# Performance work log

Measured on AMD Instinct MI355X. Metric: run time of the kernel, lower is better.

Reference implementation:

```python
import jax, jax.numpy as jnp
import numpy as np

B, S, D, H = 2, 2048, 1024, 16
DK = D // H
EPS = 1e-5


def setup_inputs() -> dict:
    key = jax.random.key(0)
    ks = jax.random.split(key, 6)
    std = (2.0 / (D + D)) ** 0.5
    return {
        "x": jax.random.normal(ks[0], (B, S, D), dtype=jnp.float32),
        "W_Q": jax.random.normal(ks[1], (D, D), dtype=jnp.float32) * std,
        "W_K": jax.random.normal(ks[2], (D, D), dtype=jnp.float32) * std,
        "W_V": jax.random.normal(ks[3], (D, D), dtype=jnp.float32) * std,
        "W_O": jax.random.normal(ks[4], (D, D), dtype=jnp.float32) * std,
        "gain": jnp.ones((D,), dtype=jnp.float32),
        "positions": jnp.arange(S, dtype=jnp.int64 if jax.config.jax_enable_x64 else jnp.int32),
        "theta": 10000,
        "max_seq_len": 2048,
    }


def rmsnorm(x, gain):
    xf = x.astype(jnp.float32)
    rms = jnp.sqrt(jnp.mean(xf * xf, axis=-1, keepdims=True) + EPS)
    return ((xf / rms) * gain).astype(x.dtype)


def apply_rope(x, sin, cos):
    # x: [..., seq, dk]; sin/cos: [seq, dk//2] broadcast over leading dims
    x_even = x[..., 0::2]
    x_odd = x[..., 1::2]
    r_even = x_even * cos - x_odd * sin
    r_odd = x_odd * cos + x_even * sin
    return jnp.stack([r_even, r_odd], axis=-1).reshape(x.shape)


def reference(x, W_Q, W_K, W_V, W_O, gain, positions, theta, max_seq_len):
    seq_len = x.shape[-2]
    Q = jnp.einsum('od,bsd->bso', W_Q, x)
    K = jnp.einsum('od,bsd->bso', W_K, x)
    V = jnp.einsum('od,bsd->bso', W_V, x)
    # RMSNorm over full d_model BEFORE head split (as in original)
    Q = rmsnorm(Q, gain)
    K = rmsnorm(K, gain)
    # split heads: [b, h, s, dk]
    Q = Q.reshape(*Q.shape[:-1], H, DK).swapaxes(-3, -2)
    K = K.reshape(*K.shape[:-1], H, DK).swapaxes(-3, -2)
    V = V.reshape(*V.shape[:-1], H, DK).swapaxes(-3, -2)
    # RoPE tables
    exponents = 2.0 * jnp.arange(DK // 2, dtype=jnp.float32) / DK
    inv_freq = 1.0 / (jnp.float32(theta) ** exponents)
    angles = positions.astype(jnp.float32)[:, None] * inv_freq[None, :]  # [S, DK//2]
    sin, cos = jnp.sin(angles), jnp.cos(angles)
    Q = apply_rope(Q, sin, cos)
    K = apply_rope(K, sin, cos)
    # causal attention
    scores = jnp.einsum('bhqd,bhkd->bhqk', Q, K) / jnp.sqrt(jnp.float32(DK))
    causal = jnp.tril(jnp.ones((seq_len, seq_len), dtype=bool))
    scores = jnp.where(causal, scores, -jnp.inf)
    attn = jax.nn.softmax(scores, axis=-1)
    out = jnp.einsum('bhqk,bhkd->bhqd', attn, V)
    out = out.swapaxes(-3, -2).reshape(*x.shape[:-1], D)
    return jnp.einsum('of,bsf->bso', W_O, out)
```

## Files before the change

kernel.cpp:

```cpp
#include <hip/hip_runtime.h>
#include <hip/hip_bf16.h>

typedef __attribute__((ext_vector_type(8))) __bf16 bf16x8;
typedef __attribute__((ext_vector_type(4))) __bf16 bf16x4;
typedef __attribute__((ext_vector_type(4))) float  f32x4;

#define S_LEN 2048
#define D_DIM 1024
#define NH    16
#define GK    1024
#define GN    1024

__device__ __forceinline__ float fast_exp2(float x) {
#if __has_builtin(__builtin_amdgcn_exp2f)
  return __builtin_amdgcn_exp2f(x);
#else
  return exp2f(x);
#endif
}

__device__ __forceinline__ void gld_lds16(const void* g, void* l) {
  __builtin_amdgcn_global_load_lds(
      (const __attribute__((address_space(1))) unsigned int*)g,
      (__attribute__((address_space(3))) unsigned int*)l, 16, 0, 0);
}

__global__ __launch_bounds__(256) void cast_all(
    const float* __restrict__ x,  const float* __restrict__ wq, const float* __restrict__ wk,
    const float* __restrict__ wv, const float* __restrict__ wo,
    __bf16* __restrict__ xb, __bf16* __restrict__ wqb, __bf16* __restrict__ wkb,
    __bf16* __restrict__ wvb, __bf16* __restrict__ wob)
{
  const int NTOT = 2 << 20;
  for (int i = blockIdx.x * 256 + threadIdx.x; i < NTOT; i += 1024 * 256) {
    const float* s; __bf16* d; int off;
    if (i < (1 << 20)) { s = x; d = xb; off = i; }
    else {
      const int j = i - (1 << 20);
      const int r = j >> 18; off = j & ((1 << 18) - 1);
      s = (r == 0) ? wq : (r == 1) ? wk : (r == 2) ? wv : wo;
      d = (r == 0) ? wqb : (r == 1) ? wkb : (r == 2) ? wvb : wob;
    }
    float4 v = ((const float4*)s)[off];
    bf16x4 o = { (__bf16)v.x, (__bf16)v.y, (__bf16)v.z, (__bf16)v.w };
    ((bf16x4*)d)[off] = o;
  }
}

__global__ __launch_bounds__(256) void gemm_bt(
    const __bf16* __restrict__ A,
    const __bf16* __restrict__ W0, const __bf16* __restrict__ W1, const __bf16* __restrict__ W2,
    __bf16* __restrict__ C0, __bf16* __restrict__ C1, __bf16* __restrict__ VtOut)
{
  const int mode = blockIdx.z;
  const __bf16* Wm = (mode == 0) ? W0 : (mode == 1) ? W1 : W2;

  __shared__ __align__(16) __bf16 As[128 * 64];
  __shared__ __align__(16) __bf16 Bs[128 * 64];

  const int tid  = threadIdx.x;
  const int lane = tid & 63;
  const int w    = tid >> 6;
  const int wr   = w >> 1, wc = w & 1;
  const int lm   = lane & 15, qd = lane >> 4;
  const int m0 = blockIdx.y * 128, n0 = blockIdx.x * 128;

  const __bf16* ap[4]; const __bf16* bp[4]; int lo[4];
  #pragma unroll
  for (int j = 0; j < 4; j++) {
    const int c = tid + 256 * j;
    const int r = c >> 3, cpos = c & 7;
    const int g = (cpos ^ (r & 7)) * 8;
    ap[j] = A  + (size_t)(m0 + r) * GK + g;
    bp[j] = Wm + (size_t)(n0 + r) * GK + g;
    lo[j] = c * 8;
  }

  const int sw = lm & 7;

  f32x4 zero = {0.f, 0.f, 0.f, 0.f};
  f32x4 acc[4][4];
  #pragma unroll
  for (int i = 0; i < 4; i++)
    #pragma unroll
    for (int j = 0; j < 4; j++) acc[i][j] = zero;

  for (int k0 = 0; k0 < GK; k0 += 64) {
    #pragma unroll
    for (int j = 0; j < 4; j++) {
      gld_lds16(ap[j] + k0, &As[lo[j]]);
      gld_lds16(bp[j] + k0, &Bs[lo[j]]);
    }
    __syncthreads();
    #pragma unroll
    for (int half = 0; half < 2; half++) {
      const int cph = ((qd + 4 * half) ^ sw) * 8;
      bf16x8 af[4], bfv[4];
      #pragma unroll
      for (int i = 0; i < 4; i++) af[i]  = *(const bf16x8*)&As[(wr * 64 + i * 16 + lm) * 64 + cph];
      #pragma unroll
      for (int j = 0; j < 4; j++) bfv[j] = *(const bf16x8*)&Bs[(wc * 64 + j * 16 + lm) * 64 + cph];
      #pragma unroll
      for (int i = 0; i < 4; i++)
        #pragma unroll
        for (int j = 0; j < 4; j++)
          acc[i][j] = __builtin_amdgcn_mfma_f32_16x16x32_bf16(af[i], bfv[j], acc[i][j], 0, 0, 0);
    }
    __syncthreads();
  }

  if (mode < 2) {
    __bf16* C = (mode == 0) ? C0 : C1;
    #pragma unroll
    for (int i = 0; i < 4; i++) {
      const int row = m0 + wr * 64 + i * 16 + qd * 4;
      #pragma unroll
      for (int j = 0; j < 4; j++) {
        const int col = n0 + wc * 64 + j * 16 + lm;
        #pragma unroll
        for (int r = 0; r < 4; r++)
          C[(size_t)(row + r) * GN + col] = (__bf16)acc[i][j][r];
      }
    }
  } else {
    #pragma unroll
    for (int i = 0; i < 4; i++) {
      const int row = m0 + wr * 64 + i * 16 + qd * 4;
      const int b = row >> 11, s = row & (S_LEN - 1);
      #pragma unroll
      for (int j = 0; j < 4; j++) {
        const int col = n0 + wc * 64 + j * 16 + lm;
        const int h = col >> 6, d = col & 63;
        bf16x4 o = { (__bf16)acc[i][j][0], (__bf16)acc[i][j][1],
                     (__bf16)acc[i][j][2], (__bf16)acc[i][j][3] };
        *(bf16x4*)(VtOut + (((size_t)(b * NH + h) * 64 + d) * S_LEN + s)) = o;
      }
    }
  }
}

__global__ __launch_bounds__(256) void gemm_out64(
    const __bf16* __restrict__ A, const __bf16* __restrict__ Wm, float* __restrict__ C)
{
  __shared__ __align__(16) __bf16 As[64 * 64];
  __shared__ __align__(16) __bf16 Bs[128 * 64];

  const int tid  = threadIdx.x;
  const int lane = tid & 63;
  const int w    = tid >> 6;
  const int wr   = w >> 1, wc = w & 1;
  const int lm   = lane & 15, qd = lane >> 4;
  const int m0 = blockIdx.y * 64, n0 = blockIdx.x * 128;

  const __bf16* ap[2]; int loA[2];
  #pragma unroll
  for (int j = 0; j < 2; j++) {
    const int c = tid + 256 * j;
    const int r = c >> 3, cpos = c & 7;
    ap[j] = A + (size_t)(m0 + r) * GK + (cpos ^ (r & 7)) * 8;
    loA[j] = c * 8;
  }
  const __bf16* bp[4]; int loB[4];
  #pragma unroll
  for (int j = 0; j < 4; j++) {
    const int c = tid + 256 * j;
    const int r = c >> 3, cpos = c & 7;
    bp[j] = Wm + (size_t)(n0 + r) * GK + (cpos ^ (r & 7)) * 8;
    loB[j] = c * 8;
  }

  const int sw = lm & 7;

  f32x4 zero = {0.f, 0.f, 0.f, 0.f};
  f32x4 acc[2][4];
  #pragma unroll
  for (int i = 0; i < 2; i++)
    #pragma unroll
    for (int j = 0; j < 4; j++) acc[i][j] = zero;

  for (int k0 = 0; k0 < GK; k0 += 64) {
    #pragma unroll
    for (int j = 0; j < 2; j++) gld_lds16(ap[j] + k0, &As[loA[j]]);
    #pragma unroll
    for (int j = 0; j < 4; j++) gld_lds16(bp[j] + k0, &Bs[loB[j]]);
    __syncthreads();
    #pragma unroll
    for (int half = 0; half < 2; half++) {
      const int cph = ((qd + 4 * half) ^ sw) * 8;
      bf16x8 af[2], bfv[4];
      #pragma unroll
      for (int i = 0; i < 2; i++) af[i]  = *(const bf16x8*)&As[(wr * 32 + i * 16 + lm) * 64 + cph];
      #pragma unroll
      for (int j = 0; j < 4; j++) bfv[j] = *(const bf16x8*)&Bs[(wc * 64 + j * 16 + lm) * 64 + cph];
      #pragma unroll
      for (int i = 0; i < 2; i++)
        #pragma unroll
        for (int j = 0; j < 4; j++)
          acc[i][j] = __builtin_amdgcn_mfma_f32_16x16x32_bf16(af[i], bfv[j], acc[i][j], 0, 0, 0);
    }
    __syncthreads();
  }

  #pragma unroll
  for (int i = 0; i < 2; i++) {
    const int row = m0 + wr * 32 + i * 16 + qd * 4;
    #pragma unroll
    for (int j = 0; j < 4; j++) {
      const int col = n0 + wc * 64 + j * 16 + lm;
      #pragma unroll
      for (int r = 0; r < 4; r++)
        C[(size_t)(row + r) * GN + col] = acc[i][j][r];
    }
  }
}

__global__ __launch_bounds__(256) void norm_rope(
    const __bf16* __restrict__ Qf, const __bf16* __restrict__ Kf,
    const float* __restrict__ gain, const int* __restrict__ positions,
    const int* __restrict__ theta_p,
    __bf16* __restrict__ Qh, __bf16* __restrict__ Kh)
{
  const int row = blockIdx.x;
  const int s = row & (S_LEN - 1), b = row >> 11;
  const int t = threadIdx.x, d0 = t * 4;

  const bf16x4 qv = *(const bf16x4*)(Qf + (size_t)row * D_DIM + d0);
  const bf16x4 kv = *(const bf16x4*)(Kf + (size_t)row * D_DIM + d0);
  const float q0 = (float)qv[0], q1 = (float)qv[1], q2 = (float)qv[2], q3 = (float)qv[3];
  const float k0 = (float)kv[0], k1 = (float)kv[1], k2 = (float)kv[2], k3 = (float)kv[3];

  float sq = q0 * q0 + q1 * q1 + q2 * q2 + q3 * q3;
  float sk = k0 * k0 + k1 * k1 + k2 * k2 + k3 * k3;
  #pragma unroll
  for (int off = 32; off; off >>= 1) { sq += __shfl_xor(sq, off); sk += __shfl_xor(sk, off); }
  __shared__ float red[8];
  const int lane = t & 63, wv = t >> 6;
  if (lane == 0) { red[wv] = sq; red[4 + wv] = sk; }
  __syncthreads();
  sq = red[0] + red[1] + red[2] + red[3];
  sk = red[4] + red[5] + red[6] + red[7];
  const float invq = rsqrtf(sq * (1.0f / 1024.0f) + 1e-5f);
  const float invk = rsqrtf(sk * (1.0f / 1024.0f) + 1e-5f);

  const float4 g = *(const float4*)(gain + d0);
  const float qn0 = q0 * invq * g.x, qn1 = q1 * invq * g.y;
  const float qn2 = q2 * invq * g.z, qn3 = q3 * invq * g.w;
  const float kn0 = k0 * invk * g.x, kn1 = k1 * invk * g.y;
  const float kn2 = k2 * invk * g.z, kn3 = k3 * invk * g.w;

  const float pos = (float)positions[s];
  const float th  = (float)theta_p[0];
  const int idx = d0 & 63, h = d0 >> 6, p0 = idx >> 1;
  const float lg32 = __log2f(th) * (1.0f / 32.0f);
  const float f0 = fast_exp2(-(float)p0 * lg32);
  const float f1 = fast_exp2(-(float)(p0 + 1) * lg32);
  float s0, cc0, s1, cc1;
  __sincosf(pos * f0, &s0, &cc0);
  __sincosf(pos * f1, &s1, &cc1);

  const float qe0 = qn0 * cc0 - qn1 * s0, qo0 = qn1 * cc0 + qn0 * s0;
  const float qe1 = qn2 * cc1 - qn3 * s1, qo1 = qn3 * cc1 + qn2 * s1;
  const float ke0 = kn0 * cc0 - kn1 * s0, ko0 = kn1 * cc0 + kn0 * s0;
  const float ke1 = kn2 * cc1 - kn3 * s1, ko1 = kn3 * cc1 + kn2 * s1;

  const size_t obase = ((size_t)((b * NH + h) * S_LEN + s)) * 64 + idx;
  bf16x4 qo = { (__bf16)qe0, (__bf16)qo0, (__bf16)qe1, (__bf16)qo1 };
  bf16x4 ko = { (__bf16)ke0, (__bf16)ko0, (__bf16)ke1, (__bf16)ko1 };
  *(bf16x4*)(Qh + obase) = qo;
  *(bf16x4*)(Kh + obase) = ko;
}

__global__ __launch_bounds__(256) void attn_fwd(
    const __bf16* __restrict__ Qh, const __bf16* __restrict__ Kh,
    const __bf16* __restrict__ Vt, __bf16* __restrict__ Ob)
{
  const int bid = blockIdx.x + 16 * blockIdx.y;
  const int px  = bid >> 5;
  const int rr  = bid & 31;
  const int bh  = (rr & 7) * 4 + (rr >> 3);
  const int tid = threadIdx.x, lane = tid & 63, w = tid >> 6;
  const int lm = lane & 15, qd = lane >> 4;

  __shared__ __align__(16) __bf16 smem[2 * 4096 + 2 * 4096 + 4 * 1152];
  __bf16* Ks = smem;
  __bf16* Vs = smem + 8192;
  __bf16* Pw = smem + 16384 + w * 1152;

  const int qtA = px, qtB = 31 - px;
  const int rowA = qtA * 64 + w * 16, rowB = qtB * 64 + w * 16;

  const size_t qbase = (size_t)bh * S_LEN * 64;
  const bf16x8 aqA0 = *(const bf16x8*)(Qh + qbase + (size_t)(rowA + lm) * 64 + qd * 8);
  const bf16x8 aqA1 = *(const bf16x8*)(Qh + qbase + (size_t)(rowA + lm) * 64 + 32 + qd * 8);
  const bf16x8 aqB0 = *(const bf16x8*)(Qh + qbase + (size_t)(rowB + lm) * 64 + qd * 8);
  const bf16x8 aqB1 = *(const bf16x8*)(Qh + qbase + (size_t)(rowB + lm) * 64 + 32 + qd * 8);

  const __bf16* Kb = Kh + (size_t)bh * S_LEN * 64;
  const __bf16* Vb = Vt + (size_t)bh * 64 * S_LEN;
  const int c0 = tid, c1 = 256 + tid;
  const int kr0 = c0 >> 3, kr1 = c1 >> 3;
  const int kg0 = ((c0 & 7) ^ (kr0 & 7)) * 8;
  const int kg1 = ((c1 & 7) ^ (kr1 & 7)) * 8;
  const int cpA = (qd ^ (lm & 7)) * 8;
  const int cpB = cpA ^ 32;

  auto stage = [&](int buf, int k0) {
    __bf16* Kd = Ks + buf * 4096;
    __bf16* Vd = Vs + buf * 4096;
    gld_lds16(Kb + (size_t)(k0 + kr0) * 64 + kg0, &Kd[c0 * 8]);
    gld_lds16(Kb + (size_t)(k0 + kr1) * 64 + kg1, &Kd[c1 * 8]);
    gld_lds16(Vb + (size_t)kr0 * S_LEN + k0 + kg0, &Vd[c0 * 8]);
    gld_lds16(Vb + (size_t)kr1 * S_LEN + k0 + kg1, &Vd[c1 * 8]);
  };

  const float SC2 = 0.125f * 1.44269504089f;
  const float OFF = 12.0f;
  f32x4 zero = {0.f, 0.f, 0.f, 0.f};
  float l[4];
  f32x4 o[4];

  stage(0, 0);

  const int b = bh >> 4, h = bh & 15;

  for (int it = 0; it < 33; ++it) {
    const int seg = (it > qtA);
    const int kt  = seg ? it - qtA - 1 : it;
    const int qt  = seg ? qtB : qtA;
    const int cur = it & 1;

    if (kt == 0) {
      #pragma unroll
      for (int r = 0; r < 4; r++) l[r] = 0.f;
      #pragma unroll
      for (int jb = 0; jb < 4; jb++) o[jb] = zero;
    }

    __syncthreads();
    if (it + 1 < 33) {
      const int nkt = (it + 1 > qtA) ? it - qtA : it + 1;
      stage(cur ^ 1, nkt * 64);
    }

    const __bf16* Kc = Ks + cur * 4096;
    const __bf16* Vc = Vs + cur * 4096;
    const bf16x8 a0 = seg ? aqB0 : aqA0;
    const bf16x8 a1 = seg ? aqB1 : aqA1;
    const int rowg = (seg ? rowB : rowA) + qd * 4;
    const int k0 = kt * 64;

    float p[4][4];
    const bool diag = (kt == qt);
    #pragma unroll
    for (int kb = 0; kb < 4; kb++) {
      const int krow = (kb * 16 + lm) * 64;
      const bf16x8 bk0 = *(const bf16x8*)&Kc[krow + cpA];
      const bf16x8 bk1 = *(const bf16x8*)&Kc[krow + cpB];
      f32x4 sc = zero;
      sc = __builtin_amdgcn_mfma_f32_16x16x32_bf16(a0, bk0, sc, 0, 0, 0);
      sc = __builtin_amdgcn_mfma_f32_16x16x32_bf16(a1, bk1, sc, 0, 0, 0);
      if (diag) {
        const int colg = k0 + kb * 16 + lm;
        #pragma unroll
        for (int r = 0; r < 4; r++) {
          const float e = fast_exp2(fmaf(sc[r], SC2, -OFF));
          p[kb][r] = (colg <= rowg + r) ? e : 0.f;
          l[r] += p[kb][r];
        }
      } else {
        #pragma unroll
        for (int r = 0; r < 4; r++) {
          p[kb][r] = fast_exp2(fmaf(sc[r], SC2, -OFF));
          l[r] += p[kb][r];
        }
      }
    }

    #pragma unroll
    for (int kb = 0; kb < 4; kb++)
      #pragma unroll
      for (int r = 0; r < 4; r++)
        Pw[(qd * 4 + r) * 72 + kb * 16 + lm] = (__bf16)p[kb][r];

    const bf16x8 ap0 = *(const bf16x8*)&Pw[lm * 72 + qd * 8];
    const bf16x8 ap1 = *(const bf16x8*)&Pw[lm * 72 + 32 + qd * 8];
    #pragma unroll
    for (int jb = 0; jb < 4; jb++) {
      const int vrow = (jb * 16 + lm) * 64;
      const bf16x8 bv0 = *(const bf16x8*)&Vc[vrow + cpA];
      const bf16x8 bv1 = *(const bf16x8*)&Vc[vrow + cpB];
      o[jb] = __builtin_amdgcn_mfma_f32_16x16x32_bf16(ap1, bv1,
              __builtin_amdgcn_mfma_f32_16x16x32_bf16(ap0, bv0, o[jb], 0, 0, 0), 0, 0, 0);
    }

    if (kt == qt) {
      #pragma unroll
      for (int r = 0; r < 4; r++) {
        float lr = l[r];
        #pragma unroll
        for (int off = 8; off; off >>= 1) lr += __shfl_xor(lr, off);
        const float inv = 1.0f / lr;
        const size_t base = ((size_t)(b * S_LEN + rowg + r)) * D_DIM + h * 64;
        #pragma unroll
        for (int jb = 0; jb < 4; jb++)
          Ob[base + jb * 16 + lm] = (__bf16)(o[jb][r] * inv);
      }
    }
  }
}

extern "C" void kernel_launch(void* const* d_in, const int* in_sizes, int n_in,
                              void* d_out, int out_size, void* d_ws, size_t ws_size,
                              hipStream_t stream)
{
  (void)in_sizes; (void)n_in; (void)out_size; (void)ws_size;
  const float* x    = (const float*)d_in[0];
  const float* WQ   = (const float*)d_in[1];
  const float* WK   = (const float*)d_in[2];
  const float* WV   = (const float*)d_in[3];
  const float* WO   = (const float*)d_in[4];
  const float* gain = (const float*)d_in[5];
  const int* positions = (const int*)d_in[6];
  const int* theta     = (const int*)d_in[7];
  float* out = (float*)d_out;

  char* ws = (char*)d_ws;
  const size_t MB = 1024 * 1024;
  __bf16* xb  = (__bf16*)(ws + 0);
  __bf16* WQb = (__bf16*)(ws + 8  * MB);
  __bf16* WKb = (__bf16*)(ws + 10 * MB);
  __bf16* WVb = (__bf16*)(ws + 12 * MB);
  __bf16* WOb = (__bf16*)(ws + 14 * MB);
  __bf16* Qfb = (__bf16*)(ws + 16 * MB);
  __bf16* Kfb = (__bf16*)(ws + 24 * MB);
  __bf16* Vt  = (__bf16*)(ws + 32 * MB);
  __bf16* Qh  = (__bf16*)(ws + 40 * MB);
  __bf16* Kh  = (__bf16*)(ws + 48 * MB);
  __bf16* Ob  = (__bf16*)(ws + 56 * MB);

  cast_all<<<1024, 256, 0, stream>>>(x, WQ, WK, WV, WO, xb, WQb, WKb, WVb, WOb);
  gemm_bt<<<dim3(8, 32, 3), 256, 0, stream>>>(xb, WQb, WKb, WVb, Qfb, Kfb, Vt);
  norm_rope<<<4096, 256, 0, stream>>>(Qfb, Kfb, gain, positions, theta, Qh, Kh);
  attn_fwd<<<dim3(16, 32), 256, 0, stream>>>(Qh, Kh, Vt, Ob);
  gemm_out64<<<dim3(8, 64), 256, 0, stream>>>(Ob, WOb, out);
}
```

Baseline: 203.1 us.

## Split paired causal query tiles into one block per tile with longest-first order

```diff
diff --git a/kernel.cpp b/kernel.cpp
--- a/kernel.cpp
+++ b/kernel.cpp
@@ -274,26 +274,23 @@
     const __bf16* __restrict__ Qh, const __bf16* __restrict__ Kh,
     const __bf16* __restrict__ Vt, __bf16* __restrict__ Ob)
 {
-  const int bid = blockIdx.x + 16 * blockIdx.y;
-  const int px  = bid >> 5;
+  const int bid = blockIdx.x;
+  const int g   = bid >> 5, gj = g & 7, gs = g >> 3;
+  const int qt  = (gs == 0) ? 31 - gj : (gs == 1) ? gj : (gs == 2) ? 23 - gj : 8 + gj;
   const int rr  = bid & 31;
   const int bh  = (rr & 7) * 4 + (rr >> 3);
   const int tid = threadIdx.x, lane = tid & 63, w = tid >> 6;
   const int lm = lane & 15, qd = lane >> 4;
 
-  __shared__ __align__(16) __bf16 smem[2 * 4096 + 2 * 4096 + 4 * 1152];
+  __shared__ __align__(16) __bf16 smem[8192 + 8192 + 4096];
   __bf16* Ks = smem;
   __bf16* Vs = smem + 8192;
-  __bf16* Pw = smem + 16384 + w * 1152;
-
-  const int qtA = px, qtB = 31 - px;
-  const int rowA = qtA * 64 + w * 16, rowB = qtB * 64 + w * 16;
-
+  __bf16* Pw = smem + 16384 + w * 1024;
+
+  const int row0 = qt * 64 + w * 16;
   const size_t qbase = (size_t)bh * S_LEN * 64;
-  const bf16x8 aqA0 = *(const bf16x8*)(Qh + qbase + (size_t)(rowA + lm) * 64 + qd * 8);
-  const bf16x8 aqA1 = *(const bf16x8*)(Qh + qbase + (size_t)(rowA + lm) * 64 + 32 + qd * 8);
-  const bf16x8 aqB0 = *(const bf16x8*)(Qh + qbase + (size_t)(rowB + lm) * 64 + qd * 8);
-  const bf16x8 aqB1 = *(const bf16x8*)(Qh + qbase + (size_t)(rowB + lm) * 64 + 32 + qd * 8);
+  const bf16x8 aq0 = *(const bf16x8*)(Qh + qbase + (size_t)(row0 + lm) * 64 + qd * 8);
+  const bf16x8 aq1 = *(const bf16x8*)(Qh + qbase + (size_t)(row0 + lm) * 64 + 32 + qd * 8);
 
   const __bf16* Kb = Kh + (size_t)bh * S_LEN * 64;
   const __bf16* Vb = Vt + (size_t)bh * 64 * S_LEN;
@@ -316,37 +313,23 @@
   const float SC2 = 0.125f * 1.44269504089f;
   const float OFF = 12.0f;
   f32x4 zero = {0.f, 0.f, 0.f, 0.f};
-  float l[4];
+  float l[4] = {0.f, 0.f, 0.f, 0.f};
   f32x4 o[4];
+  #pragma unroll
+  for (int jb = 0; jb < 4; jb++) o[jb] = zero;
 
   stage(0, 0);
 
-  const int b = bh >> 4, h = bh & 15;
-
-  for (int it = 0; it < 33; ++it) {
-    const int seg = (it > qtA);
-    const int kt  = seg ? it - qtA - 1 : it;
-    const int qt  = seg ? qtB : qtA;
-    const int cur = it & 1;
-
-    if (kt == 0) {
-      #pragma unroll
-      for (int r = 0; r < 4; r++) l[r] = 0.f;
-      #pragma unroll
-      for (int jb = 0; jb < 4; jb++) o[jb] = zero;
-    }
-
+  const int rowg = row0 + qd * 4;
+  const int pxor = qd * 4;
+
+  for (int kt = 0; kt <= qt; ++kt) {
+    const int cur = kt & 1;
     __syncthreads();
-    if (it + 1 < 33) {
-      const int nkt = (it + 1 > qtA) ? it - qtA : it + 1;
-      stage(cur ^ 1, nkt * 64);
-    }
+    if (kt < qt) stage(cur ^ 1, (kt + 1) * 64);
 
     const __bf16* Kc = Ks + cur * 4096;
     const __bf16* Vc = Vs + cur * 4096;
-    const bf16x8 a0 = seg ? aqB0 : aqA0;
-    const bf16x8 a1 = seg ? aqB1 : aqA1;
-    const int rowg = (seg ? rowB : rowA) + qd * 4;
     const int k0 = kt * 64;
 
     float p[4][4];
@@ -357,8 +340,8 @@
       const bf16x8 bk0 = *(const bf16x8*)&Kc[krow + cpA];
       const bf16x8 bk1 = *(const bf16x8*)&Kc[krow + cpB];
       f32x4 sc = zero;
-      sc = __builtin_amdgcn_mfma_f32_16x16x32_bf16(a0, bk0, sc, 0, 0, 0);
-      sc = __builtin_amdgcn_mfma_f32_16x16x32_bf16(a1, bk1, sc, 0, 0, 0);
+      sc = __builtin_amdgcn_mfma_f32_16x16x32_bf16(aq0, bk0, sc, 0, 0, 0);
+      sc = __builtin_amdgcn_mfma_f32_16x16x32_bf16(aq1, bk1, sc, 0, 0, 0);
       if (diag) {
         const int colg = k0 + kb * 16 + lm;
         #pragma unroll
@@ -377,13 +360,17 @@
     }
 
     #pragma unroll
-    for (int kb = 0; kb < 4; kb++)
-      #pragma unroll
-      for (int r = 0; r < 4; r++)
-        Pw[(qd * 4 + r) * 72 + kb * 16 + lm] = (__bf16)p[kb][r];
-
-    const bf16x8 ap0 = *(const bf16x8*)&Pw[lm * 72 + qd * 8];
-    const bf16x8 ap1 = *(const bf16x8*)&Pw[lm * 72 + 32 + qd * 8];
+    for (int kb = 0; kb < 4; kb++) {
+      const int cb = kb * 2 + (lm >> 3), wi = lm & 7;
+      #pragma unroll
+      for (int r = 0; r < 4; r++) {
+        const int prow = pxor + r;
+        Pw[prow * 64 + ((cb ^ (prow & 7)) << 3) + wi] = (__bf16)p[kb][r];
+      }
+    }
+
+    const bf16x8 ap0 = *(const bf16x8*)&Pw[lm * 64 + cpA];
+    const bf16x8 ap1 = *(const bf16x8*)&Pw[lm * 64 + cpB];
     #pragma unroll
     for (int jb = 0; jb < 4; jb++) {
       const int vrow = (jb * 16 + lm) * 64;
@@ -392,20 +379,19 @@
       o[jb] = __builtin_amdgcn_mfma_f32_16x16x32_bf16(ap1, bv1,
               __builtin_amdgcn_mfma_f32_16x16x32_bf16(ap0, bv0, o[jb], 0, 0, 0), 0, 0, 0);
     }
-
-    if (kt == qt) {
-      #pragma unroll
-      for (int r = 0; r < 4; r++) {
-        float lr = l[r];
-        #pragma unroll
-        for (int off = 8; off; off >>= 1) lr += __shfl_xor(lr, off);
-        const float inv = 1.0f / lr;
-        const size_t base = ((size_t)(b * S_LEN + rowg + r)) * D_DIM + h * 64;
-        #pragma unroll
-        for (int jb = 0; jb < 4; jb++)
-          Ob[base + jb * 16 + lm] = (__bf16)(o[jb][r] * inv);
-      }
-    }
+  }
+
+  const int b = bh >> 4, h = bh & 15;
+  #pragma unroll
+  for (int r = 0; r < 4; r++) {
+    float lr = l[r];
+    #pragma unroll
+    for (int off = 8; off; off >>= 1) lr += __shfl_xor(lr, off);
+    const float inv = 1.0f / lr;
+    const size_t base = ((size_t)(b * S_LEN + rowg + r)) * D_DIM + h * 64;
+    #pragma unroll
+    for (int jb = 0; jb < 4; jb++)
+      Ob[base + jb * 16 + lm] = (__bf16)(o[jb][r] * inv);
   }
 }
 
@@ -441,6 +427,6 @@
   cast_all<<<1024, 256, 0, stream>>>(x, WQ, WK, WV, WO, xb, WQb, WKb, WVb, WOb);
   gemm_bt<<<dim3(8, 32, 3), 256, 0, stream>>>(xb, WQb, WKb, WVb, Qfb, Kfb, Vt);
   norm_rope<<<4096, 256, 0, stream>>>(Qfb, Kfb, gain, positions, theta, Qh, Kh);
-  attn_fwd<<<dim3(16, 32), 256, 0, stream>>>(Qh, Kh, Vt, Ob);
+  attn_fwd<<<1024, 256, 0, stream>>>(Qh, Kh, Vt, Ob);
   gemm_out64<<<dim3(8, 64), 256, 0, stream>>>(Ob, WOb, out);
 }
```

New measurement: 190.8 us. 6.1% less time.
